# Performance work log

Measured on AMD Instinct MI355X. Metric: run time of the kernel, lower is better.

Reference implementation:

```python
import jax, jax.numpy as jnp
import numpy as np

B, N, M, F, K = 32, 256, 64, 128, 64
N_INTERACT_RES, N_ATOM_RES = 3, 2


def ssp(x):
    # shifted softplus, PhysNet activation
    return jax.nn.softplus(x) - jnp.log(2.0).astype(x.dtype)


def res_block(h, W1, b1, W2, b2):
    # PhysNet residual layer: h + W2 @ ssp(W1 @ ssp(h) + b1) + b2
    t = ssp(h)
    t = ssp(t @ W1.T + b1)
    return h + t @ W2.T + b2


def setup_inputs() -> dict:
    key = jax.random.key(0)
    ks = jax.random.split(key, 20)
    sF = 1.0 / np.sqrt(F)
    sK = 1.0 / np.sqrt(K)
    return {
        "x": jax.random.normal(ks[0], (B, N, F), jnp.float32),
        "rbf": jax.random.uniform(ks[1], (B, N, M, K), jnp.float32),
        "neighbor": jax.random.randint(ks[2], (B, N, M), 0, N, jnp.int32),
        "k2f_W": jax.random.normal(ks[3], (F, K), jnp.float32) * sK,  # no bias
        "Wi": jax.random.normal(ks[4], (F, F), jnp.float32) * sF,
        "bi": jnp.zeros((F,), jnp.float32),
        "ires_W1": jax.random.normal(ks[5], (N_INTERACT_RES, F, F), jnp.float32) * sF,
        "ires_b1": jnp.zeros((N_INTERACT_RES, F), jnp.float32),
        "ires_W2": jax.random.normal(ks[6], (N_INTERACT_RES, F, F), jnp.float32) * sF,
        "ires_b2": jnp.zeros((N_INTERACT_RES, F), jnp.float32),
        "Wint": jax.random.normal(ks[7], (F, F), jnp.float32) * sF,
        "bint": jnp.zeros((F,), jnp.float32),
        "u_gate": jnp.ones((F,), jnp.float32),
        "ares_W1": jax.random.normal(ks[8], (N_ATOM_RES, F, F), jnp.float32) * sF,
        "ares_b1": jnp.zeros((N_ATOM_RES, F), jnp.float32),
        "ares_W2": jax.random.normal(ks[9], (N_ATOM_RES, F, F), jnp.float32) * sF,
        "ares_b2": jnp.zeros((N_ATOM_RES, F), jnp.float32),
    }


def reference(x, rbf, neighbor, k2f_W, Wi, bi, ires_W1, ires_b1, ires_W2, ires_b2,
              Wint, bint, u_gate, ares_W1, ares_b1, ares_W2, ares_b2):
    b, n, f = x.shape
    m = neighbor.shape[2]
    xa = ssp(x)                                            # (B,N,F)
    g = jnp.einsum('bnmk,fk->bnmf', rbf, k2f_W)            # RBF filter (B,N,M,F)
    xi = ssp(xa @ Wi.T + bi)                               # self message
    # gather neighbor features: xj[b,n,m,:] = xa[b, neighbor[b,n,m], :]
    idx = jnp.broadcast_to(neighbor.reshape(b, n * m)[:, :, None], (b, n * m, f))
    xj = jnp.take_along_axis(xa, idx, axis=1).reshape(b, n, m, f)
    xj = jnp.sum(xj * g, axis=2)                           # aggregate over neighbors
    v = xi + xj
    for l in range(ires_W1.shape[0]):
        v = res_block(v, ires_W1[l], ires_b1[l], ires_W2[l], ires_b2[l])
    v = ssp(v)
    out = u_gate * x + (v @ Wint.T + bint)
    for l in range(ares_W1.shape[0]):
        out = res_block(out, ares_W1[l], ares_b1[l], ares_W2[l], ares_b2[l])
    return out
```

## Files before the change

### kernel.cpp

```cpp
#include <hip/hip_runtime.h>
#include <math.h>

#define PB 32
#define PN 256
#define PM 64
#define PF 128
#define PK 64
#define ROWS (PB*PN)
#define NTOT (ROWS*PF)

#define OFF_K2F  0
#define OFF_WI   8192
#define OFF_IW1  24576
#define OFF_IW2  73728
#define OFF_WINT 122880
#define OFF_AW1  139264
#define OFF_AW2  172032
#define TOTAL_W  204800

#define XPITCH 136

#define APB 32

typedef __attribute__((ext_vector_type(4))) float  floatx4;
typedef __attribute__((ext_vector_type(8))) short  shortx8;

__device__ __forceinline__ unsigned short f2b(float f){
    union { float f; unsigned int i; } c; c.f = f;
    unsigned int x = c.i;
    return (unsigned short)((x + 0x7fffu + ((x >> 16) & 1u)) >> 16);
}
__device__ __forceinline__ float bf2f(unsigned short u){
    union { unsigned int i; float f; } c; c.i = ((unsigned int)u) << 16; return c.f;
}
__device__ __forceinline__ float sspf(float x){
    return fmaxf(x, 0.0f) + log1pf(expf(-fabsf(x))) - 0.69314718055994531f;
}
__device__ __forceinline__ shortx8 pack8(float4 a, float4 b){
    shortx8 r;
    r[0]=(short)f2b(a.x); r[1]=(short)f2b(a.y); r[2]=(short)f2b(a.z); r[3]=(short)f2b(a.w);
    r[4]=(short)f2b(b.x); r[5]=(short)f2b(b.y); r[6]=(short)f2b(b.z); r[7]=(short)f2b(b.w);
    return r;
}

__global__ __launch_bounds__(256) void k_pre(const float* __restrict__ x,
                                             const float* __restrict__ k2f,
                                             const float* __restrict__ Wi,
                                             const float* __restrict__ iW1,
                                             const float* __restrict__ iW2,
                                             const float* __restrict__ Wint,
                                             const float* __restrict__ aW1,
                                             const float* __restrict__ aW2,
                                             float* __restrict__ xa_f,
                                             unsigned short* __restrict__ xa_b,
                                             unsigned short* __restrict__ Wb){
    int i = blockIdx.x * 256 + threadIdx.x;
    if (i < NTOT){
        float v = sspf(x[i]);
        xa_f[i] = v;
        xa_b[i] = f2b(v);
        return;
    }
    int j = i - NTOT;
    if (j >= TOTAL_W) return;
    float v;
    if      (j < OFF_WI)   v = k2f[j - OFF_K2F];
    else if (j < OFF_IW1)  v = Wi[j - OFF_WI];
    else if (j < OFF_IW2)  v = iW1[j - OFF_IW1];
    else if (j < OFF_WINT) v = iW2[j - OFF_IW2];
    else if (j < OFF_AW1)  v = Wint[j - OFF_WINT];
    else if (j < OFF_AW2)  v = aW1[j - OFF_AW1];
    else                   v = aW2[j - OFF_AW2];
    Wb[j] = f2b(v);
}

__global__ __launch_bounds__(512) void k_msg(const float* __restrict__ rbf,
                                             const int* __restrict__ nbr,
                                             const unsigned short* __restrict__ Wk2f,
                                             const float* __restrict__ xa_f,
                                             float* __restrict__ xj){
    const int tid  = threadIdx.x;
    const int w    = tid >> 6;
    const int lane = tid & 63;
    const int quad = lane >> 4;
    const int l16  = lane & 15;
    const int slot = w >> 2;
    const int t    = w & 3;

    const int blk   = blockIdx.x;
    const int b     = blk >> 3;
    const int n0    = (blk & 7) * APB;
    const int atom0 = b * PN + n0;

    __shared__ float xa_s[PN * PF];
    __shared__ float red[2][2][4][PF];

    const int rowoff = (t*16 + l16) * PK + quad*8;
    {
    }
    const float* rb0 = rbf + (size_t)(atom0 + slot) * (PM*PK) + rowoff;
    float4 r0 = *(const float4*)(rb0);
    float4 r1 = *(const float4*)(rb0 + 4);
    float4 r2 = *(const float4*)(rb0 + 32);
    float4 r3 = *(const float4*)(rb0 + 36);
    int4  nb  = *(const int4*)(nbr + (size_t)(atom0 + slot)*PM + t*16 + quad*4);

    const float* src = xa_f + (size_t)b * (PN*PF);
    #pragma unroll
    for (int p = 0; p < 16; ++p){
        int idx = p*2048 + tid*4;
        *(float4*)(&xa_s[idx]) = *(const float4*)(src + idx);
    }

    shortx8 bf0[8], bf1[8];
    #pragma unroll
    for (int ft = 0; ft < 8; ++ft){
        const unsigned short* wrow = Wk2f + (size_t)(ft*16 + l16) * PK;
        bf0[ft] = *(const shortx8*)(wrow + quad*8);
        bf1[ft] = *(const shortx8*)(wrow + 32 + quad*8);
    }

    __syncthreads();

    for (int it = 0; it < APB/2; ++it){
        const int a = slot + it*2;

        shortx8 af0 = pack8(r0, r1);
        shortx8 af1 = pack8(r2, r3);
        const int j0 = nb.x, j1 = nb.y, j2 = nb.z, j3 = nb.w;

        if (it + 1 < APB/2){
            const float* rbn = rbf + (size_t)(atom0 + a + 2) * (PM*PK) + rowoff;
            r0 = *(const float4*)(rbn);
            r1 = *(const float4*)(rbn + 4);
            r2 = *(const float4*)(rbn + 32);
            r3 = *(const float4*)(rbn + 36);
            nb = *(const int4*)(nbr + (size_t)(atom0 + a + 2)*PM + t*16 + quad*4);
        }

        floatx4 acc8[8];
        #pragma unroll
        for (int ft = 0; ft < 8; ++ft){
            floatx4 c = {0.f, 0.f, 0.f, 0.f};
            c = __builtin_amdgcn_mfma_f32_16x16x32_bf16(af0, bf0[ft], c, 0, 0, 0);
            c = __builtin_amdgcn_mfma_f32_16x16x32_bf16(af1, bf1[ft], c, 0, 0, 0);
            acc8[ft] = c;
        }

        const float* rp0 = xa_s + (size_t)j0*PF + l16;
        const float* rp1 = xa_s + (size_t)j1*PF + l16;
        const float* rp2 = xa_s + (size_t)j2*PF + l16;
        const float* rp3 = xa_s + (size_t)j3*PF + l16;
        float s[8];
        #pragma unroll
        for (int ft = 0; ft < 8; ++ft){
            float v =  acc8[ft][0] * rp0[ft*16];
            v       += acc8[ft][1] * rp1[ft*16];
            v       += acc8[ft][2] * rp2[ft*16];
            v       += acc8[ft][3] * rp3[ft*16];
            s[ft] = v;
        }

        #pragma unroll
        for (int ft = 0; ft < 8; ++ft){
            float v = s[ft];
            v += __shfl_xor(v, 16, 64);
            v += __shfl_xor(v, 32, 64);
            if (quad == 0) red[it & 1][slot][t][ft*16 + l16] = v;
        }
        __syncthreads();

        if (t == 0){
            const float* rd = &red[it & 1][slot][0][0];
            float2 v0 = *(const float2*)(rd + 0*PF + 2*lane);
            float2 v1 = *(const float2*)(rd + 1*PF + 2*lane);
            float2 v2 = *(const float2*)(rd + 2*PF + 2*lane);
            float2 v3 = *(const float2*)(rd + 3*PF + 2*lane);
            float2 o;
            o.x = v0.x + v1.x + v2.x + v3.x;
            o.y = v0.y + v1.y + v2.y + v3.y;
            *(float2*)(xj + (size_t)(atom0 + a)*PF + 2*lane) = o;
        }
    }
}

__device__ __forceinline__ void gemm2(const unsigned short* __restrict__ W,
                                      int l16, int quad, int ftbase,
                                      const shortx8 a[4], floatx4 acc[2]){
    #pragma unroll
    for (int f = 0; f < 2; ++f){
        const unsigned short* wrow = W + (size_t)((ftbase+f)*16 + l16) * PF;
        floatx4 c = {0.f, 0.f, 0.f, 0.f};
        #pragma unroll
        for (int ks = 0; ks < 4; ++ks){
            shortx8 bf = *(const shortx8*)(wrow + ks*32 + quad*8);
            c = __builtin_amdgcn_mfma_f32_16x16x32_bf16(a[ks], bf, c, 0, 0, 0);
        }
        acc[f] = c;
    }
}

__device__ __forceinline__ void relayout(unsigned short* Tls,
                                         const unsigned short t16[8],
                                         int l16, int quad, int ftbase,
                                         shortx8 a[4]){
    #pragma unroll
    for (int f = 0; f < 2; ++f)
        #pragma unroll
        for (int r = 0; r < 4; ++r)
            Tls[(quad*4 + r)*XPITCH + (ftbase+f)*16 + l16] = t16[f*4 + r];
    __syncthreads();
    #pragma unroll
    for (int ks = 0; ks < 4; ++ks)
        a[ks] = *(const shortx8*)(Tls + l16*XPITCH + ks*32 + quad*8);
}

__global__ __launch_bounds__(256) void k_chain(const unsigned short* __restrict__ xa_b,
                                               const float* __restrict__ xj,
                                               const float* __restrict__ x,
                                               const unsigned short* __restrict__ Wb,
                                               const float* __restrict__ bi,
                                               const float* __restrict__ ib1,
                                               const float* __restrict__ ib2,
                                               const float* __restrict__ bint,
                                               const float* __restrict__ ugate,
                                               const float* __restrict__ ab1,
                                               const float* __restrict__ ab2,
                                               float* __restrict__ out){
    const int tid  = threadIdx.x;
    const int wave = tid >> 6;
    const int lane = tid & 63;
    const int quad = lane >> 4;
    const int l16  = lane & 15;
    const int ftb  = wave*2;
    const int row0 = blockIdx.x * 16;

    __shared__ unsigned short Tls[2][16 * XPITCH];
    int p = 0;

    int col[2];
    #pragma unroll
    for (int f = 0; f < 2; ++f) col[f] = (ftb+f)*16 + l16;

    const unsigned short* inrow = xa_b + (size_t)(row0 + l16) * PF;
    shortx8 a[4];
    #pragma unroll
    for (int ks = 0; ks < 4; ++ks)
        a[ks] = *(const shortx8*)(inrow + ks*32 + quad*8);

    floatx4 acc[2];
    float V[8];
    unsigned short t16[8];

    gemm2(Wb + OFF_WI, l16, quad, ftb, a, acc);
    #pragma unroll
    for (int f = 0; f < 2; ++f)
        #pragma unroll
        for (int r = 0; r < 4; ++r){
            size_t idx = (size_t)(row0 + quad*4 + r)*PF + col[f];
            float of = sspf(acc[f][r] + bi[col[f]]) + xj[idx];
            V[f*4+r] = of;
            t16[f*4+r] = f2b(sspf(of));
        }
    relayout(Tls[p], t16, l16, quad, ftb, a); p ^= 1;

    for (int l = 0; l < 3; ++l){
        gemm2(Wb + OFF_IW1 + l*PF*PF, l16, quad, ftb, a, acc);
        #pragma unroll
        for (int f = 0; f < 2; ++f)
            #pragma unroll
            for (int r = 0; r < 4; ++r)
                t16[f*4+r] = f2b(sspf(acc[f][r] + ib1[l*PF + col[f]]));
        relayout(Tls[p], t16, l16, quad, ftb, a); p ^= 1;

        gemm2(Wb + OFF_IW2 + l*PF*PF, l16, quad, ftb, a, acc);
        #pragma unroll
        for (int f = 0; f < 2; ++f)
            #pragma unroll
            for (int r = 0; r < 4; ++r){
                V[f*4+r] += acc[f][r] + ib2[l*PF + col[f]];
                t16[f*4+r] = f2b(sspf(V[f*4+r]));
            }
        relayout(Tls[p], t16, l16, quad, ftb, a); p ^= 1;
    }

    gemm2(Wb + OFF_WINT, l16, quad, ftb, a, acc);
    #pragma unroll
    for (int f = 0; f < 2; ++f)
        #pragma unroll
        for (int r = 0; r < 4; ++r){
            size_t idx = (size_t)(row0 + quad*4 + r)*PF + col[f];
            float o = ugate[col[f]] * x[idx] + acc[f][r] + bint[col[f]];
            V[f*4+r] = o;
            t16[f*4+r] = f2b(sspf(o));
        }
    relayout(Tls[p], t16, l16, quad, ftb, a); p ^= 1;

    #pragma unroll
    for (int l = 0; l < 2; ++l){
        gemm2(Wb + OFF_AW1 + l*PF*PF, l16, quad, ftb, a, acc);
        #pragma unroll
        for (int f = 0; f < 2; ++f)
            #pragma unroll
            for (int r = 0; r < 4; ++r)
                t16[f*4+r] = f2b(sspf(acc[f][r] + ab1[l*PF + col[f]]));
        relayout(Tls[p], t16, l16, quad, ftb, a); p ^= 1;

        gemm2(Wb + OFF_AW2 + l*PF*PF, l16, quad, ftb, a, acc);
        if (l == 0){
            #pragma unroll
            for (int f = 0; f < 2; ++f)
                #pragma unroll
                for (int r = 0; r < 4; ++r){
                    V[f*4+r] += acc[f][r] + ab2[l*PF + col[f]];
                    t16[f*4+r] = f2b(sspf(V[f*4+r]));
                }
            relayout(Tls[p], t16, l16, quad, ftb, a); p ^= 1;
        } else {
            #pragma unroll
            for (int f = 0; f < 2; ++f)
                #pragma unroll
                for (int r = 0; r < 4; ++r){
                    size_t idx = (size_t)(row0 + quad*4 + r)*PF + col[f];
                    out[idx] = V[f*4+r] + acc[f][r] + ab2[l*PF + col[f]];
                }
        }
    }
}

extern "C" void kernel_launch(void* const* d_in, const int* in_sizes, int n_in,
                              void* d_out, int out_size, void* d_ws, size_t ws_size,
                              hipStream_t stream){
    const float* x     = (const float*)d_in[0];
    const float* rbf   = (const float*)d_in[1];
    const int*   nbr   = (const int*)d_in[2];
    const float* k2fW  = (const float*)d_in[3];
    const float* Wi    = (const float*)d_in[4];
    const float* bi    = (const float*)d_in[5];
    const float* iW1   = (const float*)d_in[6];
    const float* ib1   = (const float*)d_in[7];
    const float* iW2   = (const float*)d_in[8];
    const float* ib2   = (const float*)d_in[9];
    const float* Wint  = (const float*)d_in[10];
    const float* bint  = (const float*)d_in[11];
    const float* ugate = (const float*)d_in[12];
    const float* aW1   = (const float*)d_in[13];
    const float* ab1   = (const float*)d_in[14];
    const float* aW2   = (const float*)d_in[15];
    const float* ab2   = (const float*)d_in[16];

    char* ws = (char*)d_ws;
    unsigned short* xa_b = (unsigned short*)ws;
    float*          xa_f = (float*)(ws + (2ull  << 20));
    float*          xj   = (float*)(ws + (6ull  << 20));
    unsigned short* Wb   = (unsigned short*)(ws + (10ull << 20));

    k_pre<<<(NTOT + TOTAL_W + 255)/256, 256, 0, stream>>>(
        x, k2fW, Wi, iW1, iW2, Wint, aW1, aW2, xa_f, xa_b, Wb);
    k_msg<<<PB * (PN/APB), 512, 0, stream>>>(rbf, nbr, Wb + OFF_K2F, xa_f, xj);
    k_chain<<<ROWS/16, 256, 0, stream>>>(xa_b, xj, x, Wb,
                                         bi, ib1, ib2, bint, ugate, ab1, ab2,
                                         (float*)d_out);
}
```

Measured before the change: 288.1 us.

## Restructure message kernel per-wave, prefetch next weights, use fast exp/log in ssp

The message kernel now gives each wave four whole atoms, accumulating all 64 neighbours in registers. This removes the per-iteration shared-memory reduction and __syncthreads, and a padded LDS pitch reduces bank conflicts on the gathered rows. The dense chain kernel double-buffers weight fragments in registers, loading the next layer's weights before the current MFMA, to hide global load latency. The shifted softplus uses the hardware exp2/log intrinsics in place of libm expf/log1pf, which costs some accuracy for small values and raises register pressure.

```diff
diff --git a/kernel.cpp b/kernel.cpp
--- a/kernel.cpp
+++ b/kernel.cpp
@@ -19,6 +19,7 @@
 #define TOTAL_W  204800
 
 #define XPITCH 136
+#define GPITCH 132
 
 #define APB 32
 
@@ -30,11 +31,11 @@
     unsigned int x = c.i;
     return (unsigned short)((x + 0x7fffu + ((x >> 16) & 1u)) >> 16);
 }
-__device__ __forceinline__ float bf2f(unsigned short u){
-    union { unsigned int i; float f; } c; c.i = ((unsigned int)u) << 16; return c.f;
-}
 __device__ __forceinline__ float sspf(float x){
-    return fmaxf(x, 0.0f) + log1pf(expf(-fabsf(x))) - 0.69314718055994531f;
+    const float LOG2E = 1.4426950408889634f;
+    const float LN2   = 0.6931471805599453f;
+    float t = __builtin_amdgcn_exp2f(-fabsf(x) * LOG2E);
+    return fmaxf(x, 0.0f) + LN2 * __builtin_amdgcn_logf(1.0f + t) - LN2;
 }
 __device__ __forceinline__ shortx8 pack8(float4 a, float4 b){
     shortx8 r;
@@ -84,32 +85,33 @@
     const int lane = tid & 63;
     const int quad = lane >> 4;
     const int l16  = lane & 15;
-    const int slot = w >> 2;
-    const int t    = w & 3;
 
     const int blk   = blockIdx.x;
     const int b     = blk >> 3;
-    const int n0    = (blk & 7) * APB;
-    const int atom0 = b * PN + n0;
-
-    __shared__ float xa_s[PN * PF];
-    __shared__ float red[2][2][4][PF];
-
-    const int rowoff = (t*16 + l16) * PK + quad*8;
+    const int atom0 = b * PN + (blk & 7) * APB;
+    const int awave = atom0 + w*4;
+
+    __shared__ float xa_s[PN * GPITCH];
+
+    const int rboff = l16 * PK + quad*8;
+    const float* rb_base = rbf + (size_t)awave * (PM*PK);
+    const int*   nb_base = nbr + (size_t)awave * PM + quad*4;
+
+    float4 pA0,pA1,pA2,pA3, pB0,pB1,pB2,pB3;
+    int4 nbA, nbB;
     {
-    }
-    const float* rb0 = rbf + (size_t)(atom0 + slot) * (PM*PK) + rowoff;
-    float4 r0 = *(const float4*)(rb0);
-    float4 r1 = *(const float4*)(rb0 + 4);
-    float4 r2 = *(const float4*)(rb0 + 32);
-    float4 r3 = *(const float4*)(rb0 + 36);
-    int4  nb  = *(const int4*)(nbr + (size_t)(atom0 + slot)*PM + t*16 + quad*4);
-
-    const float* src = xa_f + (size_t)b * (PN*PF);
-    #pragma unroll
-    for (int p = 0; p < 16; ++p){
-        int idx = p*2048 + tid*4;
-        *(float4*)(&xa_s[idx]) = *(const float4*)(src + idx);
+        const float* p0 = rb_base + rboff;
+        pA0 = *(const float4*)(p0);
+        pA1 = *(const float4*)(p0 + 4);
+        pA2 = *(const float4*)(p0 + 32);
+        pA3 = *(const float4*)(p0 + 36);
+        nbA = *(const int4*)(nb_base);
+        const float* p1 = rb_base + 16*PK + rboff;
+        pB0 = *(const float4*)(p1);
+        pB1 = *(const float4*)(p1 + 4);
+        pB2 = *(const float4*)(p1 + 32);
+        pB3 = *(const float4*)(p1 + 36);
+        nbB = *(const int4*)(nb_base + 16);
     }
 
     shortx8 bf0[8], bf1[8];
@@ -120,22 +122,44 @@
         bf1[ft] = *(const shortx8*)(wrow + 32 + quad*8);
     }
 
+    const float* src = xa_f + (size_t)b * (PN*PF);
+    #pragma unroll
+    for (int p = 0; p < 16; ++p){
+        int idx = p*2048 + tid*4;
+        int row = idx >> 7, col = idx & 127;
+        *(float4*)(&xa_s[row*GPITCH + col]) = *(const float4*)(src + idx);
+    }
     __syncthreads();
 
-    for (int it = 0; it < APB/2; ++it){
-        const int a = slot + it*2;
-
-        shortx8 af0 = pack8(r0, r1);
-        shortx8 af1 = pack8(r2, r3);
-        const int j0 = nb.x, j1 = nb.y, j2 = nb.z, j3 = nb.w;
-
-        if (it + 1 < APB/2){
-            const float* rbn = rbf + (size_t)(atom0 + a + 2) * (PM*PK) + rowoff;
-            r0 = *(const float4*)(rbn);
-            r1 = *(const float4*)(rbn + 4);
-            r2 = *(const float4*)(rbn + 32);
-            r3 = *(const float4*)(rbn + 36);
-            nb = *(const int4*)(nbr + (size_t)(atom0 + a + 2)*PM + t*16 + quad*4);
+    float s[8];
+    #pragma unroll
+    for (int it = 0; it < 16; ++it){
+        const int ai = it >> 2;
+        const int t  = it & 3;
+        (void)t;
+
+        shortx8 af0, af1; int4 nb;
+        if ((it & 1) == 0){ af0 = pack8(pA0,pA1); af1 = pack8(pA2,pA3); nb = nbA; }
+        else              { af0 = pack8(pB0,pB1); af1 = pack8(pB2,pB3); nb = nbB; }
+
+        if (it + 2 < 16){
+            const int it2 = it + 2;
+            const int ai2 = it2 >> 2, t2 = it2 & 3;
+            const float* pn = rb_base + (size_t)ai2*(PM*PK) + t2*16*PK + rboff;
+            const int4*  nn = (const int4*)(nb_base + (size_t)ai2*PM + t2*16);
+            if ((it & 1) == 0){
+                pA0 = *(const float4*)(pn);
+                pA1 = *(const float4*)(pn + 4);
+                pA2 = *(const float4*)(pn + 32);
+                pA3 = *(const float4*)(pn + 36);
+                nbA = *nn;
+            } else {
+                pB0 = *(const float4*)(pn);
+                pB1 = *(const float4*)(pn + 4);
+                pB2 = *(const float4*)(pn + 32);
+                pB3 = *(const float4*)(pn + 36);
+                nbB = *nn;
+            }
         }
 
         floatx4 acc8[8];
@@ -147,55 +171,46 @@
             acc8[ft] = c;
         }
 
-        const float* rp0 = xa_s + (size_t)j0*PF + l16;
-        const float* rp1 = xa_s + (size_t)j1*PF + l16;
-        const float* rp2 = xa_s + (size_t)j2*PF + l16;
-        const float* rp3 = xa_s + (size_t)j3*PF + l16;
-        float s[8];
+        const float* rp0 = xa_s + (size_t)nb.x*GPITCH + l16;
+        const float* rp1 = xa_s + (size_t)nb.y*GPITCH + l16;
+        const float* rp2 = xa_s + (size_t)nb.z*GPITCH + l16;
+        const float* rp3 = xa_s + (size_t)nb.w*GPITCH + l16;
         #pragma unroll
         for (int ft = 0; ft < 8; ++ft){
             float v =  acc8[ft][0] * rp0[ft*16];
             v       += acc8[ft][1] * rp1[ft*16];
             v       += acc8[ft][2] * rp2[ft*16];
             v       += acc8[ft][3] * rp3[ft*16];
-            s[ft] = v;
-        }
-
-        #pragma unroll
-        for (int ft = 0; ft < 8; ++ft){
-            float v = s[ft];
-            v += __shfl_xor(v, 16, 64);
-            v += __shfl_xor(v, 32, 64);
-            if (quad == 0) red[it & 1][slot][t][ft*16 + l16] = v;
-        }
-        __syncthreads();
-
-        if (t == 0){
-            const float* rd = &red[it & 1][slot][0][0];
-            float2 v0 = *(const float2*)(rd + 0*PF + 2*lane);
-            float2 v1 = *(const float2*)(rd + 1*PF + 2*lane);
-            float2 v2 = *(const float2*)(rd + 2*PF + 2*lane);
-            float2 v3 = *(const float2*)(rd + 3*PF + 2*lane);
-            float2 o;
-            o.x = v0.x + v1.x + v2.x + v3.x;
-            o.y = v0.y + v1.y + v2.y + v3.y;
-            *(float2*)(xj + (size_t)(atom0 + a)*PF + 2*lane) = o;
-        }
-    }
-}
-
-__device__ __forceinline__ void gemm2(const unsigned short* __restrict__ W,
-                                      int l16, int quad, int ftbase,
-                                      const shortx8 a[4], floatx4 acc[2]){
+            if (t == 0) s[ft] = v; else s[ft] += v;
+        }
+
+        if (t == 3){
+            #pragma unroll
+            for (int ft = 0; ft < 8; ++ft){
+                float v = s[ft];
+                v += __shfl_xor(v, 16, 64);
+                v += __shfl_xor(v, 32, 64);
+                if (quad == 0) xj[(size_t)(awave + ai)*PF + ft*16 + l16] = v;
+            }
+        }
+    }
+}
+
+__device__ __forceinline__ void lw8(const unsigned short* __restrict__ W,
+                                    int l16, int quad, int ftb, shortx8 wf[8]){
+    #pragma unroll
+    for (int f = 0; f < 2; ++f)
+        #pragma unroll
+        for (int ks = 0; ks < 4; ++ks)
+            wf[f*4+ks] = *(const shortx8*)(W + (size_t)((ftb+f)*16 + l16)*PF + ks*32 + quad*8);
+}
+__device__ __forceinline__ void gemm2p(const shortx8 wf[8], const shortx8 a[4], floatx4 acc[2]){
     #pragma unroll
     for (int f = 0; f < 2; ++f){
-        const unsigned short* wrow = W + (size_t)((ftbase+f)*16 + l16) * PF;
         floatx4 c = {0.f, 0.f, 0.f, 0.f};
         #pragma unroll
-        for (int ks = 0; ks < 4; ++ks){
-            shortx8 bf = *(const shortx8*)(wrow + ks*32 + quad*8);
-            c = __builtin_amdgcn_mfma_f32_16x16x32_bf16(a[ks], bf, c, 0, 0, 0);
-        }
+        for (int ks = 0; ks < 4; ++ks)
+            c = __builtin_amdgcn_mfma_f32_16x16x32_bf16(a[ks], wf[f*4+ks], c, 0, 0, 0);
         acc[f] = c;
     }
 }
@@ -248,11 +263,15 @@
     for (int ks = 0; ks < 4; ++ks)
         a[ks] = *(const shortx8*)(inrow + ks*32 + quad*8);
 
+    shortx8 wA[8], wB[8];
+    lw8(Wb + OFF_WI, l16, quad, ftb, wA);
+
     floatx4 acc[2];
     float V[8];
     unsigned short t16[8];
 
-    gemm2(Wb + OFF_WI, l16, quad, ftb, a, acc);
+    lw8(Wb + OFF_IW1, l16, quad, ftb, wB);
+    gemm2p(wA, a, acc);
     #pragma unroll
     for (int f = 0; f < 2; ++f)
         #pragma unroll
@@ -264,8 +283,10 @@
         }
     relayout(Tls[p], t16, l16, quad, ftb, a); p ^= 1;
 
+    #pragma unroll
     for (int l = 0; l < 3; ++l){
-        gemm2(Wb + OFF_IW1 + l*PF*PF, l16, quad, ftb, a, acc);
+        lw8(Wb + OFF_IW2 + l*PF*PF, l16, quad, ftb, wA);
+        gemm2p(wB, a, acc);
         #pragma unroll
         for (int f = 0; f < 2; ++f)
             #pragma unroll
@@ -273,7 +294,8 @@
                 t16[f*4+r] = f2b(sspf(acc[f][r] + ib1[l*PF + col[f]]));
         relayout(Tls[p], t16, l16, quad, ftb, a); p ^= 1;
 
-        gemm2(Wb + OFF_IW2 + l*PF*PF, l16, quad, ftb, a, acc);
+        lw8(Wb + (l < 2 ? OFF_IW1 + (l+1)*PF*PF : OFF_WINT), l16, quad, ftb, wB);
+        gemm2p(wA, a, acc);
         #pragma unroll
         for (int f = 0; f < 2; ++f)
             #pragma unroll
@@ -284,7 +306,8 @@
         relayout(Tls[p], t16, l16, quad, ftb, a); p ^= 1;
     }
 
-    gemm2(Wb + OFF_WINT, l16, quad, ftb, a, acc);
+    lw8(Wb + OFF_AW1, l16, quad, ftb, wA);
+    gemm2p(wB, a, acc);
     #pragma unroll
     for (int f = 0; f < 2; ++f)
         #pragma unroll
@@ -298,7 +321,8 @@
 
     #pragma unroll
     for (int l = 0; l < 2; ++l){
-        gemm2(Wb + OFF_AW1 + l*PF*PF, l16, quad, ftb, a, acc);
+        lw8(Wb + OFF_AW2 + l*PF*PF, l16, quad, ftb, wB);
+        gemm2p(wA, a, acc);
         #pragma unroll
         for (int f = 0; f < 2; ++f)
             #pragma unroll
@@ -306,7 +330,8 @@
                 t16[f*4+r] = f2b(sspf(acc[f][r] + ab1[l*PF + col[f]]));
         relayout(Tls[p], t16, l16, quad, ftb, a); p ^= 1;
 
-        gemm2(Wb + OFF_AW2 + l*PF*PF, l16, quad, ftb, a, acc);
+        if (l == 0) lw8(Wb + OFF_AW1 + PF*PF, l16, quad, ftb, wA);
+        gemm2p(wB, a, acc);
         if (l == 0){
             #pragma unroll
             for (int f = 0; f < 2; ++f)
```

Result: slower. 300.3 us (+4.2%).
